# Kernel tuning notes

Measured on AMD Instinct MI355X. Metric: run time of the kernel, lower is better.

The kernel has to match this reference:

```python
import jax, jax.numpy as jnp
import numpy as np

NUM_HEADS = 16
D_MODEL = 1024
D_QKV = 64


def _xavier(key, shape):
    # xavier normal over last two dims (fan_in = D_MODEL, fan_out = D_QKV)
    std = float(np.sqrt(2.0 / (shape[-2] + shape[-1])))
    return jax.random.normal(key, shape, dtype=jnp.float32) * std


def setup_inputs() -> dict:
    key = jax.random.key(0)
    ks = jax.random.split(key, 9)
    B, L = 4, 2048
    q = jax.random.normal(ks[0], (B, L, D_MODEL), dtype=jnp.float32)
    k = jax.random.normal(ks[1], (B, L, D_MODEL), dtype=jnp.float32)
    v = jax.random.normal(ks[2], (B, L, D_MODEL), dtype=jnp.float32)
    mask = jax.random.randint(ks[3], (B, L, L), 0, 2, dtype=jnp.int32)
    Wq = _xavier(ks[4], (NUM_HEADS, D_MODEL, D_QKV))
    Wk = _xavier(ks[5], (NUM_HEADS, D_MODEL, D_QKV))
    Wv = _xavier(ks[6], (NUM_HEADS, D_MODEL, D_QKV))
    lim = float(1.0 / np.sqrt(D_MODEL))
    Wo_w = jax.random.uniform(ks[7], (D_MODEL, D_MODEL), minval=-lim, maxval=lim, dtype=jnp.float32)
    Wo_b = jax.random.uniform(ks[8], (D_MODEL,), minval=-lim, maxval=lim, dtype=jnp.float32)
    return {"q": q, "k": k, "v": v, "mask": mask,
            "Wq": Wq, "Wk": Wk, "Wv": Wv, "Wo_w": Wo_w, "Wo_b": Wo_b}


def reference(q, k, v, mask, Wq, Wk, Wv, Wo_w, Wo_b):
    B, L, _ = q.shape
    query = jnp.einsum('blm,nmd->bnld', q, Wq)   # [B,H,L,Dq]
    key_ = jnp.einsum('blm,nmd->bnld', k, Wk)
    value = jnp.einsum('blm,nmd->bnld', v, Wv)
    scores = jnp.einsum('bnld,bnmd->bnlm', query, key_) / jnp.sqrt(
        jnp.asarray(D_QKV, dtype=query.dtype))          # [B,H,L,L]
    scores = jnp.where(mask[:, None, :, :] == 0, jnp.asarray(-1e9, scores.dtype), scores)
    attn = jax.nn.softmax(scores, axis=-1)
    out = jnp.einsum('bnlm,bnmd->bnld', attn, value)     # [B,H,L,Dq]
    out = out.transpose(0, 2, 1, 3).reshape(B, L, D_MODEL)
    return out @ Wo_w.T + Wo_b
```

## Files before the change

kernel.cpp:

```cpp
#include <hip/hip_runtime.h>
#include <stdint.h>

typedef __bf16 bf16;
typedef __bf16 bf16x8 __attribute__((ext_vector_type(8)));
typedef float  f32x4  __attribute__((ext_vector_type(4)));
typedef uint32_t u32;
typedef uint64_t u64;

#define SCALE_L2E 0.18033688011112042f

__device__ __forceinline__ void gld_lds16(const void* gsrc, void* ldst) {
  __builtin_amdgcn_global_load_lds(
      (const __attribute__((address_space(1))) void*)gsrc,
      (__attribute__((address_space(3))) void*)ldst, 16, 0, 0);
}


__global__ void cvt3(const float* __restrict__ q, const float* __restrict__ k,
                     const float* __restrict__ v, bf16* __restrict__ out) {
  const float* in = (blockIdx.z == 0) ? q : (blockIdx.z == 1) ? k : v;
  bf16* o = out + (size_t)blockIdx.z * 8388608;
  int stride = gridDim.x * blockDim.x;
  for (int i = blockIdx.x * blockDim.x + threadIdx.x; i < 1048576; i += stride) {
    const float4* p = (const float4*)(in + (size_t)i * 8);
    float4 a = p[0], b = p[1];
    bf16x8 vv;
    vv[0]=(bf16)a.x; vv[1]=(bf16)a.y; vv[2]=(bf16)a.z; vv[3]=(bf16)a.w;
    vv[4]=(bf16)b.x; vv[5]=(bf16)b.y; vv[6]=(bf16)b.z; vv[7]=(bf16)b.w;
    *(bf16x8*)(o + (size_t)i * 8) = vv;
  }
}

__global__ void pack_w(const float* __restrict__ Wq, const float* __restrict__ Wk,
                       const float* __restrict__ Wv, const float* __restrict__ Wo,
                       bf16* __restrict__ Wt) {
  int s = blockIdx.z;
  int tid = blockIdx.x * blockDim.x + threadIdx.x;
  int n = tid >> 7, kb = tid & 127;
  const float* W = (s == 0) ? Wq : (s == 1) ? Wk : (s == 2) ? Wv : Wo;
  bf16x8 v;
  if (s < 3) {
#pragma unroll
    for (int j = 0; j < 8; ++j)
      v[j] = (bf16)W[((n >> 6) << 16) + (kb * 8 + j) * 64 + (n & 63)];
  } else {
    const float4* p = (const float4*)&W[n * 1024 + kb * 8];
    float4 a = p[0], b = p[1];
    v[0]=(bf16)a.x; v[1]=(bf16)a.y; v[2]=(bf16)a.z; v[3]=(bf16)a.w;
    v[4]=(bf16)b.x; v[5]=(bf16)b.y; v[6]=(bf16)b.z; v[7]=(bf16)b.w;
  }
  *(bf16x8*)&Wt[(size_t)s * 1048576 + (size_t)n * 1024 + kb * 8] = v;
}

__global__ void pack_mask(const int* __restrict__ mask, u32* __restrict__ mbits, int total) {
  int stride = gridDim.x * blockDim.x;
  for (int idx = blockIdx.x * blockDim.x + threadIdx.x; idx < total; idx += stride) {
    int v = mask[idx];
    u64 bal = __ballot(v != 0);
    if ((threadIdx.x & 63) == 0)
      *(u64*)&mbits[idx >> 5] = bal;
  }
}

template<int EPI>
__global__ __launch_bounds__(256, 2)
void gemm_bt(const bf16* __restrict__ A, const bf16* __restrict__ Bt,
             void* __restrict__ Cout, void* __restrict__ Cout2,
             const float* __restrict__ bias,
             size_t a_bstride, size_t b_bstride, float cscale) {
  const int gx = gridDim.x;
  int lin = blockIdx.y * gx + blockIdx.x;
  int nwg = gx * gridDim.y;
  int swz = (lin & 7) * (nwg >> 3) + (lin >> 3);
  int bx = swz % gx, by = swz / gx;
  const int bz = blockIdx.z;
  A  += a_bstride * bz;
  Bt += b_bstride * bz;
  const int row0 = by * 128, col0 = bx * 128;
  bool isK = false;
  if (EPI == 0 && row0 >= 8192) { isK = true; Bt += 1048576; }

  __shared__ bf16 sA[2][4096];
  __shared__ bf16 sB[2][4096];

  const int lane = threadIdx.x & 63, w = threadIdx.x >> 6;
  const int c = lane & 15, g = lane >> 4;
  const int wr = w >> 1, wc = w & 1;

  const int u0 = w * 128 + lane;
  const int rs0 = u0 >> 2, ps0 = u0 & 3;
  const int rs1 = (u0 + 64) >> 2, ps1 = (u0 + 64) & 3;
  const bf16* Ap = A + (size_t)row0 * 1024;
  const bf16* Bp = Bt + (size_t)col0 * 1024;
  const bf16* As0 = Ap + (size_t)rs0 * 1024 + ps0 * 8;
  const bf16* As1 = Ap + (size_t)rs1 * 1024 + ps1 * 8;
  const bf16* Bs0 = Bp + (size_t)rs0 * 1024 + ps0 * 8;
  const bf16* Bs1 = Bp + (size_t)rs1 * 1024 + ps1 * 8;

  f32x4 acc[4][4] = {};

  gld_lds16(As0, (char*)&sA[0][0] + (w * 2) * 1024);
  gld_lds16(As1, (char*)&sA[0][0] + (w * 2 + 1) * 1024);
  gld_lds16(Bs0, (char*)&sB[0][0] + (w * 2) * 1024);
  gld_lds16(Bs1, (char*)&sB[0][0] + (w * 2 + 1) * 1024);

  for (int k0 = 0; k0 < 1024; k0 += 32) {
    __syncthreads();
    int cb = (k0 >> 5) & 1, nb = cb ^ 1;
    if (k0 < 992) {
      gld_lds16(As0 + k0 + 32, (char*)&sA[nb][0] + (w * 2) * 1024);
      gld_lds16(As1 + k0 + 32, (char*)&sA[nb][0] + (w * 2 + 1) * 1024);
      gld_lds16(Bs0 + k0 + 32, (char*)&sB[nb][0] + (w * 2) * 1024);
      gld_lds16(Bs1 + k0 + 32, (char*)&sB[nb][0] + (w * 2 + 1) * 1024);
    }

    bf16x8 af[4], bfr[4];
#pragma unroll
    for (int m = 0; m < 4; ++m)
      af[m] = *(const bf16x8*)&sA[cb][(wr * 64 + m * 16 + c) * 32 + g * 8];
#pragma unroll
    for (int n = 0; n < 4; ++n)
      bfr[n] = *(const bf16x8*)&sB[cb][(wc * 64 + n * 16 + c) * 32 + g * 8];
#pragma unroll
    for (int m = 0; m < 4; ++m)
#pragma unroll
      for (int n = 0; n < 4; ++n)
        acc[m][n] = __builtin_amdgcn_mfma_f32_16x16x32_bf16(af[m], bfr[n], acc[m][n], 0, 0, 0);
  }

  float csc = (EPI == 0 && isK) ? 1.0f : cscale;
#pragma unroll
  for (int m = 0; m < 4; ++m) {
    int row_base = row0 + wr * 64 + m * 16 + g * 4;
#pragma unroll
    for (int n = 0; n < 4; ++n) {
      int col = col0 + wc * 64 + n * 16 + c;
#pragma unroll
      for (int r = 0; r < 4; ++r) {
        int row = row_base + r;
        float val = acc[m][n][r];
        if (EPI == 0) {
          int rl = row & 8191;
          int b = rl >> 11, l = rl & 2047, h = col >> 6, d = col & 63;
          bf16* dst = isK ? (bf16*)Cout2 : (bf16*)Cout;
          dst[(((size_t)(b * 16 + h) * 2048 + l) << 6) + d] = (bf16)(val * csc);
        } else if (EPI == 1) {
          ((bf16*)Cout)[((size_t)(bz * 1024 + row)) * 2048 + col] = (bf16)val;
        } else {
          ((float*)Cout)[(size_t)row * 1024 + col] = val + bias[col];
        }
      }
    }
  }
}

__global__ __launch_bounds__(256, 3)
void attn_fwd(const bf16* __restrict__ Qp, const bf16* __restrict__ Kp,
              const bf16* __restrict__ Vt, const u32* __restrict__ mbits,
              bf16* __restrict__ X) {
  int lin = blockIdx.y * 16 + blockIdx.x;
  int swz = (lin & 7) * 128 + (lin >> 3);
  int qt = swz & 15, bh = swz >> 4;
  int b = bh >> 4, h = bh & 15;
  int q0 = qt * 128;

  const int tid = threadIdx.x;
  const int lane = tid & 63, w = tid >> 6;
  const int c = lane & 15, g = lane >> 4;

  __shared__ char smem[49152];
  char* sKV = smem;
  char* sPw = smem + 32768 + w * 4096;

  const int c7 = c & 7;
  const int y0 = (g ^ c7) << 4;
  const int y1 = ((4 + g) ^ c7) << 4;
  const int ko0 = c * 128 + y0;
  const int ko1 = c * 128 + y1;
  const int vo0 = 8192 + c * 128 + y0;
  const int vo1 = 8192 + c * 128 + y1;
  const char* paddr0 = sPw + c * 128 + y0;
  const char* paddr1 = sPw + c * 128 + y1;
  char* pw[4];
#pragma unroll
  for (int nk = 0; nk < 4; ++nk)
    pw[nk] = sPw + c * 128 + ((g & 1) * 8) + (((nk * 2 + (g >> 1)) ^ c7) << 4);

  const int r0 = tid >> 3, bb0 = tid & 7;
  const int r1 = (256 + tid) >> 3, bb1 = tid & 7;
  const int dK0 = r0 * 128 + ((bb0 ^ (r0 & 7)) << 4);
  const int dK1 = r1 * 128 + ((bb1 ^ (r1 & 7)) << 4);
  const int dV0 = 8192 + dK0;
  const int dV1 = 8192 + dK1;
  const bf16* gK0 = Kp + (size_t)bh * 131072 + r0 * 64 + bb0 * 8;
  const bf16* gK1 = Kp + (size_t)bh * 131072 + r1 * 64 + bb1 * 8;
  const bf16* gV0 = Vt + ((size_t)(b * 1024 + h * 64 + r0)) * 2048 + bb0 * 8;
  const bf16* gV1 = Vt + ((size_t)(b * 1024 + h * 64 + r1)) * 2048 + bb1 * 8;

  const bf16* Qbase = Qp + ((size_t)bh * 2048) * 64;
  bf16x8 qf[2][2];
#pragma unroll
  for (int nq = 0; nq < 2; ++nq) {
    int qg = q0 + w * 32 + nq * 16 + c;
#pragma unroll
    for (int kk = 0; kk < 2; ++kk)
      qf[nq][kk] = *(const bf16x8*)&Qbase[(size_t)qg * 64 + kk * 32 + g * 8];
  }

  const u64* Mrow0 = (const u64*)(mbits + ((size_t)b * 2048 + (q0 + w * 32 + c)) * 64);
  const u64* Mrow1 = (const u64*)(mbits + ((size_t)b * 2048 + (q0 + w * 32 + 16 + c)) * 64);

  f32x4 oacc[4][2] = {};
  float lrun0 = 0.f, lrun1 = 0.f;

  {
    uint4 kr0 = *(const uint4*)gK0, kr1 = *(const uint4*)gK1;
    uint4 vr0 = *(const uint4*)gV0, vr1 = *(const uint4*)gV1;
    *(uint4*)(sKV + dK0) = kr0; *(uint4*)(sKV + dK1) = kr1;
    *(uint4*)(sKV + dV0) = vr0; *(uint4*)(sKV + dV1) = vr1;
  }
  u64 mw0 = Mrow0[0], mw1 = Mrow1[0];

  for (int t = 0; t < 32; ++t) {
    __syncthreads();
    const char* kbuf = sKV + ((t & 1) << 14);

    uint4 kr0, kr1, vr0, vr1;
    u64 mn0 = 0, mn1 = 0;
    if (t < 31) {
      kr0 = *(const uint4*)(gK0 + (size_t)(t + 1) * 4096);
      kr1 = *(const uint4*)(gK1 + (size_t)(t + 1) * 4096);
      vr0 = *(const uint4*)(gV0 + (size_t)(t + 1) * 64);
      vr1 = *(const uint4*)(gV1 + (size_t)(t + 1) * 64);
      mn0 = Mrow0[t + 1];
      mn1 = Mrow1[t + 1];
    }

    f32x4 st[4][2] = {};
#pragma unroll
    for (int nk = 0; nk < 4; ++nk) {
      bf16x8 kfa = *(const bf16x8*)(kbuf + ko0 + nk * 2048);
      st[nk][0] = __builtin_amdgcn_mfma_f32_16x16x32_bf16(kfa, qf[0][0], st[nk][0], 0, 0, 0);
      st[nk][1] = __builtin_amdgcn_mfma_f32_16x16x32_bf16(kfa, qf[1][0], st[nk][1], 0, 0, 0);
      bf16x8 kfb = *(const bf16x8*)(kbuf + ko1 + nk * 2048);
      st[nk][0] = __builtin_amdgcn_mfma_f32_16x16x32_bf16(kfb, qf[0][1], st[nk][0], 0, 0, 0);
      st[nk][1] = __builtin_amdgcn_mfma_f32_16x16x32_bf16(kfb, qf[1][1], st[nk][1], 0, 0, 0);
    }

#pragma unroll
    for (int nq = 0; nq < 2; ++nq) {
      u64 ms = (nq ? mw1 : mw0) >> (4 * g);
      u32 ma = (u32)ms;
      u32 mb = (u32)(ms >> 32);
      float ls = 0.f;
#pragma unroll
      for (int nk = 0; nk < 4; ++nk) {
        u32 msel = (nk < 2) ? ma : mb;
        const int bs = (nk & 1) * 16;
#pragma unroll
        for (int tt = 0; tt < 2; ++tt) {
          float e0 = __builtin_amdgcn_exp2f(st[nk][nq][tt * 2]);
          float e1 = __builtin_amdgcn_exp2f(st[nk][nq][tt * 2 + 1]);
          e0 = (msel & (1u << (bs + tt * 2)))     ? e0 : 0.f;
          e1 = (msel & (1u << (bs + tt * 2 + 1))) ? e1 : 0.f;
          ls += e0;
          ls += e1;
          union { bf16 h2[2]; u32 uu; } pk;
          pk.h2[0] = (bf16)e0; pk.h2[1] = (bf16)e1;
          *(u32*)(pw[nk] + nq * 2048 + tt * 4) = pk.uu;
        }
      }
      if (nq) lrun1 += ls; else lrun0 += ls;
    }

#pragma unroll
    for (int kk = 0; kk < 2; ++kk) {
      const char* pa = kk ? paddr1 : paddr0;
      const int vo = kk ? vo1 : vo0;
      bf16x8 pf0 = *(const bf16x8*)(pa);
      bf16x8 pf1 = *(const bf16x8*)(pa + 2048);
#pragma unroll
      for (int md = 0; md < 4; ++md) {
        bf16x8 vf = *(const bf16x8*)(kbuf + vo + md * 2048);
        oacc[md][0] = __builtin_amdgcn_mfma_f32_16x16x32_bf16(vf, pf0, oacc[md][0], 0, 0, 0);
        oacc[md][1] = __builtin_amdgcn_mfma_f32_16x16x32_bf16(vf, pf1, oacc[md][1], 0, 0, 0);
      }
    }

    if (t < 31) {
      char* nbuf = sKV + (((t + 1) & 1) << 14);
      *(uint4*)(nbuf + dK0) = kr0; *(uint4*)(nbuf + dK1) = kr1;
      *(uint4*)(nbuf + dV0) = vr0; *(uint4*)(nbuf + dV1) = vr1;
    }
    mw0 = mn0; mw1 = mn1;
  }

  lrun0 += __shfl_xor(lrun0, 16); lrun0 += __shfl_xor(lrun0, 32);
  lrun1 += __shfl_xor(lrun1, 16); lrun1 += __shfl_xor(lrun1, 32);
  float inv0 = 1.f / lrun0;
  float inv1 = 1.f / lrun1;

  __syncthreads();
  char* Xl = smem;
#pragma unroll
  for (int nq = 0; nq < 2; ++nq) {
    float inv = nq ? inv1 : inv0;
    int ql = w * 32 + nq * 16 + c;
#pragma unroll
    for (int md = 0; md < 4; ++md)
#pragma unroll
      for (int r = 0; r < 4; ++r) {
        int d = md * 16 + g * 4 + r;
        int blk = d >> 3, off = d & 7;
        *(bf16*)(Xl + ql * 128 + ((blk ^ (ql & 7)) << 4) + off * 2) =
            (bf16)(oacc[md][nq][r] * inv);
      }
  }
  __syncthreads();
#pragma unroll
  for (int i = 0; i < 4; ++i) {
    int u = i * 256 + tid;
    int row = u >> 3, blk = u & 7;
    uint4 xv = *(const uint4*)(Xl + row * 128 + ((blk ^ (row & 7)) << 4));
    *(uint4*)&X[(size_t)(b * 2048 + q0 + row) * 1024 + h * 64 + blk * 8] = xv;
  }
}


extern "C" void kernel_launch(void* const* d_in, const int* in_sizes, int n_in,
                              void* d_out, int out_size, void* d_ws, size_t ws_size,
                              hipStream_t stream) {
  const float* q    = (const float*)d_in[0];
  const float* k    = (const float*)d_in[1];
  const float* v    = (const float*)d_in[2];
  const int*   mask = (const int*)d_in[3];
  const float* Wq   = (const float*)d_in[4];
  const float* Wk   = (const float*)d_in[5];
  const float* Wv   = (const float*)d_in[6];
  const float* Wo   = (const float*)d_in[7];
  const float* Wb   = (const float*)d_in[8];

  char* ws = (char*)d_ws;
  bf16* qb = (bf16*)(ws + 0);
  bf16* kb = (bf16*)(ws + 16777216);
  bf16* vb = (bf16*)(ws + 33554432);
  bf16* Wt = (bf16*)(ws + 50331648);
  bf16* Qp = (bf16*)(ws + 58720256);
  bf16* Kp = (bf16*)(ws + 75497472);
  bf16* Vt = (bf16*)(ws + 92274688);
  bf16* Xb = (bf16*)(ws + 109051904);
  u32*  mb = (u32*) (ws + 125829120);

  cvt3<<<dim3(512, 1, 3), 256, 0, stream>>>(q, k, v, qb);
  pack_w<<<dim3(512, 1, 4), 256, 0, stream>>>(Wq, Wk, Wv, Wo, Wt);
  pack_mask<<<2048, 256, 0, stream>>>(mask, mb, 16777216);

  gemm_bt<0><<<dim3(8, 128, 1), 256, 0, stream>>>(qb, Wt, Qp, Kp, nullptr, 0, 0, SCALE_L2E);
  gemm_bt<1><<<dim3(16, 8, 4), 256, 0, stream>>>(Wt + 2097152, vb, Vt, nullptr, nullptr, 0, 2097152, 1.0f);

  attn_fwd<<<dim3(16, 64, 1), 256, 0, stream>>>(Qp, Kp, Vt, mb, Xb);

  gemm_bt<2><<<dim3(8, 64, 1), 256, 0, stream>>>(Xb, Wt + 3145728, (float*)d_out, nullptr, Wb, 0, 0, 1.0f);
}
```

Measured before the change: 263.9 us.

## Deepen GEMM K-tile with swizzled LDS, compute softmax denominators via MFMA, add setprio

The projection GEMM now stages 64-wide K tiles into an XOR-swizzled shared-memory layout. This halves the loop iterations and barriers and is meant to avoid LDS bank conflicts. In the attention kernel, the per-row softmax sum is computed with an extra MFMA against a ones vector instead of scalar adds and shuffles. Probability stores are widened to 8-byte writes, and s_setprio raises wave priority around the MFMA blocks. The larger LDS footprint may reduce occupancy, and the bf16-rounded sums slightly change numerics.

```diff
diff --git a/kernel.cpp b/kernel.cpp
--- a/kernel.cpp
+++ b/kernel.cpp
@@ -80,52 +80,68 @@
   bool isK = false;
   if (EPI == 0 && row0 >= 8192) { isK = true; Bt += 1048576; }
 
-  __shared__ bf16 sA[2][4096];
-  __shared__ bf16 sB[2][4096];
+  __shared__ bf16 sA[2][8192];
+  __shared__ bf16 sB[2][8192];
 
   const int lane = threadIdx.x & 63, w = threadIdx.x >> 6;
   const int c = lane & 15, g = lane >> 4;
   const int wr = w >> 1, wc = w & 1;
-
-  const int u0 = w * 128 + lane;
-  const int rs0 = u0 >> 2, ps0 = u0 & 3;
-  const int rs1 = (u0 + 64) >> 2, ps1 = (u0 + 64) & 3;
+  const int c7 = c & 7;
+
+  const int ric = lane >> 3;
+  const int pblk = (lane & 7) ^ (ric & 7);
   const bf16* Ap = A + (size_t)row0 * 1024;
   const bf16* Bp = Bt + (size_t)col0 * 1024;
-  const bf16* As0 = Ap + (size_t)rs0 * 1024 + ps0 * 8;
-  const bf16* As1 = Ap + (size_t)rs1 * 1024 + ps1 * 8;
-  const bf16* Bs0 = Bp + (size_t)rs0 * 1024 + ps0 * 8;
-  const bf16* Bs1 = Bp + (size_t)rs1 * 1024 + ps1 * 8;
+  const bf16* Asrc[4];
+  const bf16* Bsrc[4];
+#pragma unroll
+  for (int ii = 0; ii < 4; ++ii) {
+    int r = 8 * (w * 4 + ii) + ric;
+    Asrc[ii] = Ap + (size_t)r * 1024 + pblk * 8;
+    Bsrc[ii] = Bp + (size_t)r * 1024 + pblk * 8;
+  }
+
+  const int y0 = (g ^ c7) << 4;
+  const int y1 = ((4 + g) ^ c7) << 4;
+  const int abase = wr * 8192 + c * 128;
+  const int bbase = wc * 8192 + c * 128;
 
   f32x4 acc[4][4] = {};
 
-  gld_lds16(As0, (char*)&sA[0][0] + (w * 2) * 1024);
-  gld_lds16(As1, (char*)&sA[0][0] + (w * 2 + 1) * 1024);
-  gld_lds16(Bs0, (char*)&sB[0][0] + (w * 2) * 1024);
-  gld_lds16(Bs1, (char*)&sB[0][0] + (w * 2 + 1) * 1024);
-
-  for (int k0 = 0; k0 < 1024; k0 += 32) {
+#pragma unroll
+  for (int ii = 0; ii < 4; ++ii) {
+    gld_lds16(Asrc[ii], (char*)&sA[0][0] + (w * 4 + ii) * 1024);
+    gld_lds16(Bsrc[ii], (char*)&sB[0][0] + (w * 4 + ii) * 1024);
+  }
+
+  for (int k0 = 0; k0 < 1024; k0 += 64) {
     __syncthreads();
-    int cb = (k0 >> 5) & 1, nb = cb ^ 1;
-    if (k0 < 992) {
-      gld_lds16(As0 + k0 + 32, (char*)&sA[nb][0] + (w * 2) * 1024);
-      gld_lds16(As1 + k0 + 32, (char*)&sA[nb][0] + (w * 2 + 1) * 1024);
-      gld_lds16(Bs0 + k0 + 32, (char*)&sB[nb][0] + (w * 2) * 1024);
-      gld_lds16(Bs1 + k0 + 32, (char*)&sB[nb][0] + (w * 2 + 1) * 1024);
-    }
-
-    bf16x8 af[4], bfr[4];
-#pragma unroll
-    for (int m = 0; m < 4; ++m)
-      af[m] = *(const bf16x8*)&sA[cb][(wr * 64 + m * 16 + c) * 32 + g * 8];
-#pragma unroll
-    for (int n = 0; n < 4; ++n)
-      bfr[n] = *(const bf16x8*)&sB[cb][(wc * 64 + n * 16 + c) * 32 + g * 8];
-#pragma unroll
-    for (int m = 0; m < 4; ++m)
+    int cb = (k0 >> 6) & 1, nb = cb ^ 1;
+    if (k0 < 960) {
+#pragma unroll
+      for (int ii = 0; ii < 4; ++ii) {
+        gld_lds16(Asrc[ii] + k0 + 64, (char*)&sA[nb][0] + (w * 4 + ii) * 1024);
+        gld_lds16(Bsrc[ii] + k0 + 64, (char*)&sB[nb][0] + (w * 4 + ii) * 1024);
+      }
+    }
+    const char* a8 = (const char*)&sA[cb][0] + abase;
+    const char* b8 = (const char*)&sB[cb][0] + bbase;
+#pragma unroll
+    for (int kk = 0; kk < 2; ++kk) {
+      const int yk = kk ? y1 : y0;
+      bf16x8 af[4], bfr[4];
+#pragma unroll
+      for (int m = 0; m < 4; ++m)
+        af[m] = *(const bf16x8*)(a8 + m * 2048 + yk);
 #pragma unroll
       for (int n = 0; n < 4; ++n)
-        acc[m][n] = __builtin_amdgcn_mfma_f32_16x16x32_bf16(af[m], bfr[n], acc[m][n], 0, 0, 0);
+        bfr[n] = *(const bf16x8*)(b8 + n * 2048 + yk);
+#pragma unroll
+      for (int m = 0; m < 4; ++m)
+#pragma unroll
+        for (int n = 0; n < 4; ++n)
+          acc[m][n] = __builtin_amdgcn_mfma_f32_16x16x32_bf16(af[m], bfr[n], acc[m][n], 0, 0, 0);
+    }
   }
 
   float csc = (EPI == 0 && isK) ? 1.0f : cscale;
@@ -207,11 +223,15 @@
       qf[nq][kk] = *(const bf16x8*)&Qbase[(size_t)qg * 64 + kk * 32 + g * 8];
   }
 
+  bf16x8 onesv;
+#pragma unroll
+  for (int i = 0; i < 8; ++i) onesv[i] = (bf16)1.0f;
+
   const u64* Mrow0 = (const u64*)(mbits + ((size_t)b * 2048 + (q0 + w * 32 + c)) * 64);
   const u64* Mrow1 = (const u64*)(mbits + ((size_t)b * 2048 + (q0 + w * 32 + 16 + c)) * 64);
 
   f32x4 oacc[4][2] = {};
-  float lrun0 = 0.f, lrun1 = 0.f;
+  f32x4 dacc[2] = {};
 
   {
     uint4 kr0 = *(const uint4*)gK0, kr1 = *(const uint4*)gK1;
@@ -237,6 +257,7 @@
     }
 
     f32x4 st[4][2] = {};
+    __builtin_amdgcn_s_setprio(1);
 #pragma unroll
     for (int nk = 0; nk < 4; ++nk) {
       bf16x8 kfa = *(const bf16x8*)(kbuf + ko0 + nk * 2048);
@@ -246,39 +267,41 @@
       st[nk][0] = __builtin_amdgcn_mfma_f32_16x16x32_bf16(kfb, qf[0][1], st[nk][0], 0, 0, 0);
       st[nk][1] = __builtin_amdgcn_mfma_f32_16x16x32_bf16(kfb, qf[1][1], st[nk][1], 0, 0, 0);
     }
+    __builtin_amdgcn_s_setprio(0);
 
 #pragma unroll
     for (int nq = 0; nq < 2; ++nq) {
       u64 ms = (nq ? mw1 : mw0) >> (4 * g);
       u32 ma = (u32)ms;
-      u32 mb = (u32)(ms >> 32);
-      float ls = 0.f;
+      u32 mb2 = (u32)(ms >> 32);
 #pragma unroll
       for (int nk = 0; nk < 4; ++nk) {
-        u32 msel = (nk < 2) ? ma : mb;
+        u32 msel = (nk < 2) ? ma : mb2;
         const int bs = (nk & 1) * 16;
-#pragma unroll
-        for (int tt = 0; tt < 2; ++tt) {
-          float e0 = __builtin_amdgcn_exp2f(st[nk][nq][tt * 2]);
-          float e1 = __builtin_amdgcn_exp2f(st[nk][nq][tt * 2 + 1]);
-          e0 = (msel & (1u << (bs + tt * 2)))     ? e0 : 0.f;
-          e1 = (msel & (1u << (bs + tt * 2 + 1))) ? e1 : 0.f;
-          ls += e0;
-          ls += e1;
-          union { bf16 h2[2]; u32 uu; } pk;
-          pk.h2[0] = (bf16)e0; pk.h2[1] = (bf16)e1;
-          *(u32*)(pw[nk] + nq * 2048 + tt * 4) = pk.uu;
-        }
-      }
-      if (nq) lrun1 += ls; else lrun0 += ls;
-    }
-
+        float e0 = __builtin_amdgcn_exp2f(st[nk][nq][0]);
+        float e1 = __builtin_amdgcn_exp2f(st[nk][nq][1]);
+        float e2 = __builtin_amdgcn_exp2f(st[nk][nq][2]);
+        float e3 = __builtin_amdgcn_exp2f(st[nk][nq][3]);
+        e0 = (msel & (1u << (bs + 0))) ? e0 : 0.f;
+        e1 = (msel & (1u << (bs + 1))) ? e1 : 0.f;
+        e2 = (msel & (1u << (bs + 2))) ? e2 : 0.f;
+        e3 = (msel & (1u << (bs + 3))) ? e3 : 0.f;
+        union { bf16 hh[4]; uint2 dd; } pk;
+        pk.hh[0] = (bf16)e0; pk.hh[1] = (bf16)e1;
+        pk.hh[2] = (bf16)e2; pk.hh[3] = (bf16)e3;
+        *(uint2*)(pw[nk] + nq * 2048) = pk.dd;
+      }
+    }
+
+    __builtin_amdgcn_s_setprio(1);
 #pragma unroll
     for (int kk = 0; kk < 2; ++kk) {
       const char* pa = kk ? paddr1 : paddr0;
       const int vo = kk ? vo1 : vo0;
       bf16x8 pf0 = *(const bf16x8*)(pa);
       bf16x8 pf1 = *(const bf16x8*)(pa + 2048);
+      dacc[0] = __builtin_amdgcn_mfma_f32_16x16x32_bf16(onesv, pf0, dacc[0], 0, 0, 0);
+      dacc[1] = __builtin_amdgcn_mfma_f32_16x16x32_bf16(onesv, pf1, dacc[1], 0, 0, 0);
 #pragma unroll
       for (int md = 0; md < 4; ++md) {
         bf16x8 vf = *(const bf16x8*)(kbuf + vo + md * 2048);
@@ -286,6 +309,7 @@
         oacc[md][1] = __builtin_amdgcn_mfma_f32_16x16x32_bf16(vf, pf1, oacc[md][1], 0, 0, 0);
       }
     }
+    __builtin_amdgcn_s_setprio(0);
 
     if (t < 31) {
       char* nbuf = sKV + (((t + 1) & 1) << 14);
@@ -295,10 +319,8 @@
     mw0 = mn0; mw1 = mn1;
   }
 
-  lrun0 += __shfl_xor(lrun0, 16); lrun0 += __shfl_xor(lrun0, 32);
-  lrun1 += __shfl_xor(lrun1, 16); lrun1 += __shfl_xor(lrun1, 32);
-  float inv0 = 1.f / lrun0;
-  float inv1 = 1.f / lrun1;
+  float inv0 = 1.f / dacc[0][0];
+  float inv1 = 1.f / dacc[1][0];
 
   __syncthreads();
   char* Xl = smem;
```

Measured after the change: 263.6 us. Within noise of the previous version (-0.1%).
